# Kernel optimization log

Hardware: AMD Instinct MI355X
Metric: run time of the kernel (lower is better)

## Reference

```python
import jax, jax.numpy as jnp
import numpy as np

MODEL_DIM = 128
NUM_HEADS = 8

def setup_inputs() -> dict:
    key = jax.random.key(0)
    kx, kq, kk, kv = jax.random.split(key, 4)
    B, S, D, H = 4, 2048, MODEL_DIM, NUM_HEADS
    scale = 1.0 / np.sqrt(D)
    x = jax.random.normal(kx, (B, S, D), dtype=jnp.float32)
    # nn.Linear weights: shape [out_features, in_features] = [H*D, D]
    W_q = jax.random.normal(kq, (H * D, D), dtype=jnp.float32) * scale
    W_k = jax.random.normal(kk, (H * D, D), dtype=jnp.float32) * scale
    W_v = jax.random.normal(kv, (H * D, D), dtype=jnp.float32) * scale
    return {"x": x, "W_q": W_q, "W_k": W_k, "W_v": W_v}

def reference(x, W_q, W_k, W_v):
    B, S, D = x.shape
    H = NUM_HEADS
    # projections: y = x @ W.T, then split heads -> [B, H, S, D]
    def proj(W):
        y = jnp.einsum('bsd,ed->bse', x, W)  # [B, S, H*D]
        return y.reshape(B, S, H, D).transpose(0, 2, 1, 3)
    Q, K, V = proj(W_q), proj(W_k), proj(W_v)
    # scores [B, H, S, S]
    A = jnp.einsum('bhsd,bhtd->bhst', Q, K) / jnp.sqrt(jnp.asarray(D, x.dtype))
    # AV then softmax over the model_dim axis (as in original: softmax after matmul)
    Z = jax.nn.softmax(jnp.einsum('bhst,bhtd->bhsd', A, V), axis=-1)
    return Z
```

## Files before the change

### kernel.cpp

```cpp
#include <hip/hip_runtime.h>
#include <hip/hip_bf16.h>


#define NB 4
#define NS 2048
#define ND 128
#define NH 8
#define EPB (NS * ND)

typedef unsigned short u16;
typedef unsigned int u32;
typedef short bf16x8 __attribute__((ext_vector_type(8)));
typedef float f32x4 __attribute__((ext_vector_type(4)));

#define MFMA(a, b, c) __builtin_amdgcn_mfma_f32_16x16x32_bf16((a), (b), (c), 0, 0, 0)

__device__ __forceinline__ void splitf(float f, u16& hi, u16& lo) {
    u32 fb = __float_as_uint(f);
    u32 hb = fb + 0x7FFFu + ((fb >> 16) & 1u);
    hi = (u16)(hb >> 16);
    float fh = __uint_as_float((hb >> 16) << 16);
    float fl = f - fh;
    u32 lb = __float_as_uint(fl);
    u32 lr = lb + 0x7FFFu + ((lb >> 16) & 1u);
    lo = (u16)(lr >> 16);
}


__global__ __launch_bounds__(256) void proj_kernel(
    const float* __restrict__ xg, const float* __restrict__ Wqg,
    const float* __restrict__ Wkg, const float* __restrict__ Wvg,
    u16* __restrict__ ws, int b0, int nbh)
{
    const int which = blockIdx.z;
    const float* __restrict__ Wt = (which == 0) ? Wqg : (which == 1) ? Wkg : Wvg;

    const int tid = threadIdx.x;
    const int wv = tid >> 6;
    const int l  = tid & 63;
    const int c  = l & 15;
    const int g  = l >> 4;
    const int wr = wv & 1;
    const int wc = wv >> 1;
    const int s0 = b0 * NS + blockIdx.x * 64 + wr * 32;
    const int e0 = blockIdx.y * 128 + wc * 64;

    f32x4 acc[2][4];
    #pragma unroll
    for (int mi = 0; mi < 2; ++mi)
        #pragma unroll
        for (int ni = 0; ni < 4; ++ni) acc[mi][ni] = (f32x4){0.f, 0.f, 0.f, 0.f};

    #pragma unroll
    for (int kc = 0; kc < 4; ++kc) {
        bf16x8 ah[2], al[2], bh[4], bl[4];
        #pragma unroll
        for (int mi = 0; mi < 2; ++mi) {
            const float* p = xg + (size_t)(s0 + mi * 16 + c) * ND + kc * 32 + g * 8;
            float4 v0 = *(const float4*)p;
            float4 v1 = *(const float4*)(p + 4);
            union { u16 u[8]; bf16x8 v; } H, L;
            float vv[8] = { v0.x, v0.y, v0.z, v0.w, v1.x, v1.y, v1.z, v1.w };
            #pragma unroll
            for (int j = 0; j < 8; ++j) splitf(vv[j], H.u[j], L.u[j]);
            ah[mi] = H.v; al[mi] = L.v;
        }
        #pragma unroll
        for (int ni = 0; ni < 4; ++ni) {
            const float* p = Wt + (size_t)(e0 + ni * 16 + c) * ND + kc * 32 + g * 8;
            float4 v0 = *(const float4*)p;
            float4 v1 = *(const float4*)(p + 4);
            union { u16 u[8]; bf16x8 v; } H, L;
            float vv[8] = { v0.x, v0.y, v0.z, v0.w, v1.x, v1.y, v1.z, v1.w };
            #pragma unroll
            for (int j = 0; j < 8; ++j) splitf(vv[j], H.u[j], L.u[j]);
            bh[ni] = H.v; bl[ni] = L.v;
        }
        #pragma unroll
        for (int mi = 0; mi < 2; ++mi)
            #pragma unroll
            for (int ni = 0; ni < 4; ++ni) {
                acc[mi][ni] = MFMA(ah[mi], bh[ni], acc[mi][ni]);
                acc[mi][ni] = MFMA(ah[mi], bl[ni], acc[mi][ni]);
                acc[mi][ni] = MFMA(al[mi], bh[ni], acc[mi][ni]);
            }
    }

    const size_t TS = (size_t)nbh * EPB;
    #pragma unroll
    for (int mi = 0; mi < 2; ++mi)
        #pragma unroll
        for (int ni = 0; ni < 4; ++ni)
            #pragma unroll
            for (int r = 0; r < 4; ++r) {
                const int sg = s0 + mi * 16 + 4 * g + r;
                const int e  = e0 + ni * 16 + c;
                const int bl_ = (sg >> 11) - b0;
                const int sl  = sg & 2047;
                const int h = e >> 7, d = e & 127;
                const size_t tb = (size_t)(bl_ * NH + h) * EPB;
                u16 ph, pl;
                splitf(acc[mi][ni][r], ph, pl);
                size_t flat;
                if (which == 0) {
                    flat = ((size_t)((sl >> 4) * 4 + (d >> 5)) * 64
                            + ((d >> 3) & 3) * 16 + (sl & 15)) * 8 + (d & 7);
                    ws[0 * TS + tb + flat] = ph;
                    ws[1 * TS + tb + flat] = pl;
                } else if (which == 1) {
                    flat = ((size_t)(((sl >> 5) * 4 + (d >> 5)) * 2 + ((sl >> 4) & 1)) * 64
                            + ((d >> 3) & 3) * 16 + (sl & 15)) * 8 + (d & 7);
                    ws[2 * TS + tb + flat] = ph;
                    ws[3 * TS + tb + flat] = pl;
                } else {
                    flat = ((size_t)((sl >> 5) * 8 + (d >> 4)) * 64
                            + ((sl >> 3) & 3) * 16 + (d & 15)) * 8 + (sl & 7);
                    ws[4 * TS + tb + flat] = ph;
                    ws[5 * TS + tb + flat] = pl;
                }
            }
}

__global__ __launch_bounds__(256, 2) void attn_kernel(
    const u16* __restrict__ ws, float* __restrict__ outg, int b0, int nbh)
{
    __shared__ __align__(16) u16 sbuf[2][4][4096];
    __shared__ u32 sP[4][32 * 17];

    const int tid = threadIdx.x;
    const int Wv = tid >> 6;
    const int l  = tid & 63;
    const int c  = l & 15;
    const int g  = l >> 4;
    const int bhl = blockIdx.y;
    const size_t tb = (size_t)bhl * EPB;
    const size_t TS = (size_t)nbh * EPB;

    const u16* QH = ws;
    const u16* QL = ws + 1 * TS;
    const u16* KH = ws + 2 * TS;
    const u16* KL = ws + 3 * TS;
    const u16* VH = ws + 4 * TS;
    const u16* VL = ws + 5 * TS;

    const int qb = blockIdx.x * 128 + Wv * 32;

    bf16x8 qh[2][4], ql[2][4];
    #pragma unroll
    for (int mi = 0; mi < 2; ++mi)
        #pragma unroll
        for (int kc = 0; kc < 4; ++kc) {
            size_t f = tb + ((size_t)(((qb + 16 * mi) >> 4) * 4 + kc) * 64 + l) * 8;
            qh[mi][kc] = *(const bf16x8*)(QH + f);
            ql[mi][kc] = *(const bf16x8*)(QL + f);
        }

    f32x4 z[2][8];
    #pragma unroll
    for (int mi = 0; mi < 2; ++mi)
        #pragma unroll
        for (int ni = 0; ni < 8; ++ni) z[mi][ni] = (f32x4){0.f, 0.f, 0.f, 0.f};

    const u16* srcs[4] = { KH, KL, VH, VL };
    auto stage = [&](int buf, int T) {
        #pragma unroll
        for (int t4 = 0; t4 < 4; ++t4)
            #pragma unroll
            for (int r = 0; r < 2; ++r)
                __builtin_amdgcn_global_load_lds(
                    (const __attribute__((address_space(1))) void*)
                        (srcs[t4] + tb + (size_t)T * 4096 + r * 2048 + tid * 8),
                    (__attribute__((address_space(3))) void*)
                        (&sbuf[buf][t4][r * 2048 + tid * 8]),
                    16, 0, 0);
    };

    u32* sPW = &sP[Wv][0];
    const float scale = 0.08838834764831845f;

    stage(0, 0);

    for (int T = 0; T < 64; ++T) {
        const int cur = T & 1;
        if (T < 63) {
            stage(cur ^ 1, T + 1);
            asm volatile("s_waitcnt vmcnt(8)" ::: "memory");
        } else {
            asm volatile("s_waitcnt vmcnt(0)" ::: "memory");
        }
        __builtin_amdgcn_s_barrier();
        asm volatile("" ::: "memory");

        const u16* bKH = &sbuf[cur][0][0];
        const u16* bKL = &sbuf[cur][1][0];
        const u16* bVH = &sbuf[cur][2][0];
        const u16* bVL = &sbuf[cur][3][0];

        f32x4 s[2][2];
        #pragma unroll
        for (int mi = 0; mi < 2; ++mi)
            #pragma unroll
            for (int nt = 0; nt < 2; ++nt) s[mi][nt] = (f32x4){0.f, 0.f, 0.f, 0.f};
        __builtin_amdgcn_s_setprio(1);
        #pragma unroll
        for (int kc = 0; kc < 4; ++kc) {
            bf16x8 kh0 = *(const bf16x8*)(bKH + ((kc * 2 + 0) * 64 + l) * 8);
            bf16x8 kh1 = *(const bf16x8*)(bKH + ((kc * 2 + 1) * 64 + l) * 8);
            bf16x8 kl0 = *(const bf16x8*)(bKL + ((kc * 2 + 0) * 64 + l) * 8);
            bf16x8 kl1 = *(const bf16x8*)(bKL + ((kc * 2 + 1) * 64 + l) * 8);
            #pragma unroll
            for (int mi = 0; mi < 2; ++mi) {
                s[mi][0] = MFMA(qh[mi][kc], kh0, s[mi][0]);
                s[mi][0] = MFMA(qh[mi][kc], kl0, s[mi][0]);
                s[mi][0] = MFMA(ql[mi][kc], kh0, s[mi][0]);
                s[mi][1] = MFMA(qh[mi][kc], kh1, s[mi][1]);
                s[mi][1] = MFMA(qh[mi][kc], kl1, s[mi][1]);
                s[mi][1] = MFMA(ql[mi][kc], kh1, s[mi][1]);
            }
        }
        __builtin_amdgcn_s_setprio(0);

        bf16x8 pa_h[2], pa_l[2];
        #pragma unroll
        for (int mi = 0; mi < 2; ++mi) {
            #pragma unroll
            for (int nt = 0; nt < 2; ++nt)
                #pragma unroll
                for (int r = 0; r < 4; ++r) {
                    float p = s[mi][nt][r] * scale;
                    u16 ph, pl; splitf(p, ph, pl);
                    sPW[(nt * 16 + c) * 17 + 4 * g + r] = (u32)ph | ((u32)pl << 16);
                }
            union { u16 uh[8]; bf16x8 v; } ph8;
            union { u16 ul[8]; bf16x8 v; } pl8;
            #pragma unroll
            for (int j = 0; j < 8; ++j) {
                u32 v = sPW[(8 * g + j) * 17 + c];
                ph8.uh[j] = (u16)(v & 0xFFFFu);
                pl8.ul[j] = (u16)(v >> 16);
            }
            pa_h[mi] = ph8.v;
            pa_l[mi] = pl8.v;
        }

        __builtin_amdgcn_s_setprio(1);
        #pragma unroll
        for (int ni = 0; ni < 8; ++ni) {
            bf16x8 vh = *(const bf16x8*)(bVH + (ni * 64 + l) * 8);
            bf16x8 vl = *(const bf16x8*)(bVL + (ni * 64 + l) * 8);
            #pragma unroll
            for (int mi = 0; mi < 2; ++mi) {
                z[mi][ni] = MFMA(pa_h[mi], vh, z[mi][ni]);
                z[mi][ni] = MFMA(pa_h[mi], vl, z[mi][ni]);
                z[mi][ni] = MFMA(pa_l[mi], vh, z[mi][ni]);
            }
        }
        __builtin_amdgcn_s_setprio(0);

        asm volatile("" ::: "memory");
        __builtin_amdgcn_s_barrier();
    }

    const size_t obase = (size_t)(b0 * NH + bhl) * EPB;
    #pragma unroll
    for (int mi = 0; mi < 2; ++mi)
        #pragma unroll
        for (int r = 0; r < 4; ++r) {
            float v[8];
            float m = -3.4e38f;
            #pragma unroll
            for (int ni = 0; ni < 8; ++ni) { v[ni] = z[mi][ni][r]; m = fmaxf(m, v[ni]); }
            #pragma unroll
            for (int off = 1; off < 16; off <<= 1) m = fmaxf(m, __shfl_xor(m, off, 64));
            float sum = 0.f;
            #pragma unroll
            for (int ni = 0; ni < 8; ++ni) { v[ni] = expf(v[ni] - m); sum += v[ni]; }
            #pragma unroll
            for (int off = 1; off < 16; off <<= 1) sum += __shfl_xor(sum, off, 64);
            const float inv = 1.f / sum;
            const int q = qb + 16 * mi + 4 * g + r;
            #pragma unroll
            for (int ni = 0; ni < 8; ++ni)
                outg[obase + (size_t)q * ND + ni * 16 + c] = v[ni] * inv;
        }
}

extern "C" void kernel_launch(void* const* d_in, const int* in_sizes, int n_in,
                              void* d_out, int out_size, void* d_ws, size_t ws_size,
                              hipStream_t stream)
{
    (void)out_size;
    int xi = 0;
    for (int i = 0; i < n_in && i < 4; ++i)
        if (in_sizes[i] == NB * NS * ND) { xi = i; break; }
    const float* x = (const float*)d_in[xi];
    const float* Wsp[3]; int w = 0;
    for (int i = 0; i < 4; ++i) if (i != xi) Wsp[w++] = (const float*)d_in[i];
    const float* Wq = Wsp[0];
    const float* Wk = Wsp[1];
    const float* Wv = Wsp[2];
    float* out = (float*)d_out;
    u16* ws = (u16*)d_ws;

    auto slice_bytes = [](int nb) { return (size_t)6 * nb * NH * EPB * 2; };
    int nb = (ws_size >= slice_bytes(4)) ? 4 : (ws_size >= slice_bytes(2)) ? 2 : 1;
    const int nbh = nb * NH;

    for (int b0 = 0; b0 < NB; b0 += nb) {
        proj_kernel<<<dim3(nb * 32, 8, 3), dim3(256), 0, stream>>>(
            x, Wq, Wk, Wv, ws, b0, nbh);
        attn_kernel<<<dim3(16, nbh), dim3(256), 0, stream>>>(
            ws, out, b0, nbh);
    }
}
```

Measured before the change: 332.4 us.

## Presplit inputs to bf16 hi/lo fragments and stage projection output through LDS

A new presplit kernel converts x and the three weight matrices once into bf16 hi/lo pairs laid out in MFMA fragment order. The projection kernel no longer repeats that split work for every tile, and it keeps the x fragments in registers across all k-chunks. Output is gathered in shared memory and written to the workspace as coalesced 16-byte stores, replacing the scattered 2-byte stores. The cost is an extra kernel launch, more workspace, and one more global round trip for the split data.

New measurement: 296.7 us. 1.12x faster.

```diff
diff --git a/kernel.cpp b/kernel.cpp
--- a/kernel.cpp
+++ b/kernel.cpp
@@ -7,11 +7,16 @@
 #define ND 128
 #define NH 8
 #define EPB (NS * ND)
+#define XFRAGS (512 * 4)
+#define WFRAGS (3 * 64 * 4)
+#define PS_ELEMS ((size_t)2 * XFRAGS * 512 + (size_t)2 * WFRAGS * 512)
 
 typedef unsigned short u16;
 typedef unsigned int u32;
 typedef short bf16x8 __attribute__((ext_vector_type(8)));
 typedef float f32x4 __attribute__((ext_vector_type(4)));
+
+struct __align__(16) us8 { u16 u[8]; };
 
 #define MFMA(a, b, c) __builtin_amdgcn_mfma_f32_16x16x32_bf16((a), (b), (c), 0, 0, 0)
 
@@ -26,15 +31,47 @@
     lo = (u16)(lr >> 16);
 }
 
-
-__global__ __launch_bounds__(256) void proj_kernel(
+__global__ __launch_bounds__(256) void presplit_kernel(
     const float* __restrict__ xg, const float* __restrict__ Wqg,
     const float* __restrict__ Wkg, const float* __restrict__ Wvg,
-    u16* __restrict__ ws, int b0, int nbh)
+    u16* __restrict__ ps)
 {
+    const int gid = blockIdx.x * 256 + threadIdx.x;
+    const int total = (XFRAGS + WFRAGS) * 64;
+    if (gid >= total) return;
+    const int fi = gid >> 6, l = gid & 63;
+    const float* src;
+    u16 *H, *L;
+    if (fi < XFRAGS) {
+        const int m16 = fi >> 2, kc = fi & 3;
+        src = xg + (size_t)(m16 * 16 + (l & 15)) * ND + kc * 32 + (l >> 4) * 8;
+        H = ps + (size_t)fi * 512 + l * 8;
+        L = H + (size_t)XFRAGS * 512;
+    } else {
+        const int wfi = fi - XFRAGS;
+        const int e16g = wfi >> 2, kc = wfi & 3;
+        const int t = e16g >> 6, e16 = e16g & 63;
+        const float* Wt = (t == 0) ? Wqg : (t == 1) ? Wkg : Wvg;
+        src = Wt + (size_t)(e16 * 16 + (l & 15)) * ND + kc * 32 + (l >> 4) * 8;
+        H = ps + (size_t)2 * XFRAGS * 512 + (size_t)wfi * 512 + l * 8;
+        L = H + (size_t)WFRAGS * 512;
+    }
+    float4 v0 = *(const float4*)src;
+    float4 v1 = *(const float4*)(src + 4);
+    float vv[8] = { v0.x, v0.y, v0.z, v0.w, v1.x, v1.y, v1.z, v1.w };
+    us8 hh, ll;
+    #pragma unroll
+    for (int j = 0; j < 8; ++j) splitf(vv[j], hh.u[j], ll.u[j]);
+    *(us8*)H = hh;
+    *(us8*)L = ll;
+}
+
+__global__ __launch_bounds__(256) void proj_kernel(
+    const u16* __restrict__ ps, u16* __restrict__ ws, int b0, int nbh)
+{
+    __shared__ u32 sE[8192];
+
     const int which = blockIdx.z;
-    const float* __restrict__ Wt = (which == 0) ? Wqg : (which == 1) ? Wkg : Wvg;
-
     const int tid = threadIdx.x;
     const int wv = tid >> 6;
     const int l  = tid & 63;
@@ -42,8 +79,27 @@
     const int g  = l >> 4;
     const int wr = wv & 1;
     const int wc = wv >> 1;
-    const int s0 = b0 * NS + blockIdx.x * 64 + wr * 32;
-    const int e0 = blockIdx.y * 128 + wc * 64;
+    const int bx = blockIdx.x;
+    const int bgl = bx >> 5;
+    const int slb = (bx & 31) * 64;
+    const int h = blockIdx.y;
+    const int m0 = (b0 + bgl) * NS + slb;
+
+    const u16* XH = ps;
+    const u16* XL = ps + (size_t)XFRAGS * 512;
+    const u16* WH = ps + (size_t)2 * XFRAGS * 512;
+    const u16* WL = WH + (size_t)WFRAGS * 512;
+
+    const int m16b = (m0 >> 4) + wr * 2;
+    bf16x8 ah[2][4], al[2][4];
+    #pragma unroll
+    for (int mi = 0; mi < 2; ++mi)
+        #pragma unroll
+        for (int kc = 0; kc < 4; ++kc) {
+            size_t f = ((size_t)(m16b + mi) * 4 + kc) * 512 + l * 8;
+            ah[mi][kc] = *(const bf16x8*)(XH + f);
+            al[mi][kc] = *(const bf16x8*)(XL + f);
+        }
 
     f32x4 acc[2][4];
     #pragma unroll
@@ -51,74 +107,67 @@
         #pragma unroll
         for (int ni = 0; ni < 4; ++ni) acc[mi][ni] = (f32x4){0.f, 0.f, 0.f, 0.f};
 
+    const int e16b = which * 64 + h * 8 + wc * 4;
     #pragma unroll
     for (int kc = 0; kc < 4; ++kc) {
-        bf16x8 ah[2], al[2], bh[4], bl[4];
-        #pragma unroll
-        for (int mi = 0; mi < 2; ++mi) {
-            const float* p = xg + (size_t)(s0 + mi * 16 + c) * ND + kc * 32 + g * 8;
-            float4 v0 = *(const float4*)p;
-            float4 v1 = *(const float4*)(p + 4);
-            union { u16 u[8]; bf16x8 v; } H, L;
-            float vv[8] = { v0.x, v0.y, v0.z, v0.w, v1.x, v1.y, v1.z, v1.w };
-            #pragma unroll
-            for (int j = 0; j < 8; ++j) splitf(vv[j], H.u[j], L.u[j]);
-            ah[mi] = H.v; al[mi] = L.v;
-        }
+        bf16x8 bh[4], bl[4];
         #pragma unroll
         for (int ni = 0; ni < 4; ++ni) {
-            const float* p = Wt + (size_t)(e0 + ni * 16 + c) * ND + kc * 32 + g * 8;
-            float4 v0 = *(const float4*)p;
-            float4 v1 = *(const float4*)(p + 4);
-            union { u16 u[8]; bf16x8 v; } H, L;
-            float vv[8] = { v0.x, v0.y, v0.z, v0.w, v1.x, v1.y, v1.z, v1.w };
-            #pragma unroll
-            for (int j = 0; j < 8; ++j) splitf(vv[j], H.u[j], L.u[j]);
-            bh[ni] = H.v; bl[ni] = L.v;
+            size_t f = ((size_t)(e16b + ni) * 4 + kc) * 512 + l * 8;
+            bh[ni] = *(const bf16x8*)(WH + f);
+            bl[ni] = *(const bf16x8*)(WL + f);
         }
         #pragma unroll
         for (int mi = 0; mi < 2; ++mi)
             #pragma unroll
             for (int ni = 0; ni < 4; ++ni) {
-                acc[mi][ni] = MFMA(ah[mi], bh[ni], acc[mi][ni]);
-                acc[mi][ni] = MFMA(ah[mi], bl[ni], acc[mi][ni]);
-                acc[mi][ni] = MFMA(al[mi], bh[ni], acc[mi][ni]);
-            }
-    }
-
-    const size_t TS = (size_t)nbh * EPB;
+                acc[mi][ni] = MFMA(ah[mi][kc], bh[ni], acc[mi][ni]);
+                acc[mi][ni] = MFMA(ah[mi][kc], bl[ni], acc[mi][ni]);
+                acc[mi][ni] = MFMA(al[mi][kc], bh[ni], acc[mi][ni]);
+            }
+    }
+
     #pragma unroll
     for (int mi = 0; mi < 2; ++mi)
         #pragma unroll
         for (int ni = 0; ni < 4; ++ni)
             #pragma unroll
             for (int r = 0; r < 4; ++r) {
-                const int sg = s0 + mi * 16 + 4 * g + r;
-                const int e  = e0 + ni * 16 + c;
-                const int bl_ = (sg >> 11) - b0;
-                const int sl  = sg & 2047;
-                const int h = e >> 7, d = e & 127;
-                const size_t tb = (size_t)(bl_ * NH + h) * EPB;
+                const int slL = wr * 32 + mi * 16 + 4 * g + r;
+                const int d   = wc * 64 + ni * 16 + c;
                 u16 ph, pl;
                 splitf(acc[mi][ni][r], ph, pl);
-                size_t flat;
-                if (which == 0) {
-                    flat = ((size_t)((sl >> 4) * 4 + (d >> 5)) * 64
-                            + ((d >> 3) & 3) * 16 + (sl & 15)) * 8 + (d & 7);
-                    ws[0 * TS + tb + flat] = ph;
-                    ws[1 * TS + tb + flat] = pl;
-                } else if (which == 1) {
-                    flat = ((size_t)(((sl >> 5) * 4 + (d >> 5)) * 2 + ((sl >> 4) & 1)) * 64
-                            + ((d >> 3) & 3) * 16 + (sl & 15)) * 8 + (d & 7);
-                    ws[2 * TS + tb + flat] = ph;
-                    ws[3 * TS + tb + flat] = pl;
-                } else {
-                    flat = ((size_t)((sl >> 5) * 8 + (d >> 4)) * 64
-                            + ((sl >> 3) & 3) * 16 + (d & 15)) * 8 + (sl & 7);
-                    ws[4 * TS + tb + flat] = ph;
-                    ws[5 * TS + tb + flat] = pl;
-                }
-            }
+                u32 off;
+                if (which == 0)
+                    off = (u32)(((slL >> 4) * 4 + (d >> 5)) * 512
+                          + ((d >> 3) & 3) * 128 + (slL & 15) * 8 + (d & 7));
+                else if (which == 1)
+                    off = (u32)(((((slL >> 5) * 4 + (d >> 5)) * 2 + ((slL >> 4) & 1)) * 512)
+                          + ((d >> 3) & 3) * 128 + (slL & 15) * 8 + (d & 7));
+                else
+                    off = (u32)(((slL >> 5) * 8 + (d >> 4)) * 512
+                          + ((slL >> 3) & 3) * 128 + (d & 15) * 8 + (slL & 7));
+                sE[off] = (u32)ph | ((u32)pl << 16);
+            }
+    __syncthreads();
+
+    const size_t TS = (size_t)nbh * EPB;
+    const size_t tb = (size_t)(bgl * NH + h) * EPB;
+    u16* HB = ws + (size_t)(2 * which) * TS + tb + (size_t)slb * 128;
+    u16* LB = HB + TS;
+    #pragma unroll
+    for (int c4 = 0; c4 < 4; ++c4) {
+        const int idx = c4 * 2048 + tid * 8;
+        us8 hh, ll;
+        #pragma unroll
+        for (int j = 0; j < 8; ++j) {
+            u32 v = sE[idx + j];
+            hh.u[j] = (u16)(v & 0xFFFFu);
+            ll.u[j] = (u16)(v >> 16);
+        }
+        *(us8*)(HB + idx) = hh;
+        *(us8*)(LB + idx) = ll;
+    }
 }
 
 __global__ __launch_bounds__(256, 2) void attn_kernel(
@@ -302,13 +351,22 @@
     float* out = (float*)d_out;
     u16* ws = (u16*)d_ws;
 
-    auto slice_bytes = [](int nb) { return (size_t)6 * nb * NH * EPB * 2; };
-    int nb = (ws_size >= slice_bytes(4)) ? 4 : (ws_size >= slice_bytes(2)) ? 2 : 1;
+    auto need_bytes = [](int nb) {
+        return ((size_t)6 * nb * NH * EPB + PS_ELEMS) * 2;
+    };
+    int nb = (ws_size >= need_bytes(4)) ? 4 : (ws_size >= need_bytes(2)) ? 2 : 1;
     const int nbh = nb * NH;
+    u16* psb = ws + (size_t)6 * nbh * EPB;
+
+    {
+        const int total = (XFRAGS + WFRAGS) * 64;
+        presplit_kernel<<<dim3((total + 255) / 256), dim3(256), 0, stream>>>(
+            x, Wq, Wk, Wv, psb);
+    }
 
     for (int b0 = 0; b0 < NB; b0 += nb) {
         proj_kernel<<<dim3(nb * 32, 8, 3), dim3(256), 0, stream>>>(
-            x, Wq, Wk, Wv, ws, b0, nbh);
+            psb, ws, b0, nbh);
         attn_kernel<<<dim3(16, nbh), dim3(256), 0, stream>>>(
             ws, out, b0, nbh);
     }
```
